# Optimization experiments

Hardware: AMD Instinct MI355X
Metric: run time of the kernel (lower is better)

Reference implementation:

```python
import jax, jax.numpy as jnp
import numpy as np

T_STEPS = 100
T_EMB = 16
EPS = 1e-8


def sin_emb(t, dim):
    # sinusoidal_time_embedding: [cos(t*f), sin(t*f)] with f = exp(-log(1e4)*i/half)
    half = dim // 2
    freqs = jnp.exp(-jnp.log(jnp.float32(10000.0)) * jnp.arange(half, dtype=jnp.float32) / half)
    a = t.astype(jnp.float32)[:, None] * freqs[None, :]
    return jnp.concatenate([jnp.cos(a), jnp.sin(a)], axis=-1)


def lstm_layer(x_tbf, W_ih, W_hh, b):
    # x_tbf: [T, B, F]; torch gate order i, f, g, o
    B = x_tbf.shape[1]
    H = W_hh.shape[1]

    def step(carry, x_t):
        h, c = carry
        g = x_t @ W_ih.T + h @ W_hh.T + b
        i, f, gg, o = jnp.split(g, 4, axis=-1)
        c = jax.nn.sigmoid(f) * c + jax.nn.sigmoid(i) * jnp.tanh(gg)
        h = jax.nn.sigmoid(o) * jnp.tanh(c)
        return (h, c), h

    z = jnp.zeros((B, H), x_tbf.dtype)
    (h, c), ys = jax.lax.scan(step, (z, z), x_tbf)
    return ys, h


def _forward(x_hist, x_future, y0, turb_idx, pred_steps, init_noise, turb_emb,
             W_ih0, W_hh0, b_ih0, b_hh0, W_ih1, W_hh1, b_ih1, b_hh1,
             W1, b1, W2, b2, W3, b3):
    betas = jnp.linspace(1e-4, 0.02, T_STEPS).astype(jnp.float32)
    alphas = 1.0 - betas
    alpha_bars = jnp.cumprod(alphas)

    B = x_hist.shape[0]
    emb = turb_emb[turb_idx]  # [B, E]
    eh = jnp.broadcast_to(emb[:, None, :], (B, x_hist.shape[1], emb.shape[1]))
    ef = jnp.broadcast_to(emb[:, None, :], (B, x_future.shape[1], emb.shape[1]))
    xh = jnp.concatenate([x_hist, eh], axis=-1).transpose(1, 0, 2)    # [T_in, B, F+E]
    xf = jnp.concatenate([x_future, ef], axis=-1).transpose(1, 0, 2)  # [P, B, exo+E]

    ys0, _ = lstm_layer(xh, W_ih0, W_hh0, b_ih0 + b_hh0)
    _, enc_out = lstm_layer(ys0, W_ih1, W_hh1, b_ih1 + b_hh1)         # [B, H] = h[-1]

    def mlp(x):
        h = jax.nn.relu(x @ W1.T + b1)
        h = jax.nn.relu(h @ W2.T + b2)
        return h @ W3.T + b3

    def ar_step(prev_y, xs):
        exo_t, step, y_init = xs
        cond = jnp.concatenate([enc_out, exo_t, prev_y], axis=1)  # [B, cond_dim]
        h_e = sin_emb(jnp.full((B,), step), T_EMB)

        def dstep(y, t):
            t_e = sin_emb(jnp.full((B,), t), T_EMB)
            eps_hat = mlp(jnp.concatenate([cond, y, t_e, h_e], axis=1))  # [B,1]
            b_t, a_t, ab_t = betas[t], alphas[t], alpha_bars[t]
            pred_x0 = (y - jnp.sqrt(1.0 - ab_t) * eps_hat) / (jnp.sqrt(ab_t) + EPS)
            mean = (y - b_t / (jnp.sqrt(1.0 - ab_t) + EPS) * eps_hat) / (jnp.sqrt(a_t) + EPS)
            # eval mode -> deterministic sampling: posterior noise term is zero
            return jnp.where(t == 0, pred_x0, mean), None

        y, _ = jax.lax.scan(dstep, y_init, jnp.arange(T_STEPS - 1, -1, -1))
        return y, y[:, 0]

    _, seq = jax.lax.scan(ar_step, y0, (xf, jnp.arange(pred_steps), init_noise))
    return seq.T[:, :, None]  # [B, pred_steps, 1]


def setup_inputs() -> dict:
    key = jax.random.key(0)
    ks = list(jax.random.split(key, 24))
    kit = iter(ks)
    B, T_IN, F_IN, EXO, EMB, PRED, HID, NTURB = 1024, 96, 8, 6, 16, 8, 128, 100
    in0 = F_IN + EMB                 # 24
    cond_dim = HID + EXO + EMB + 1   # 151
    in_mlp = cond_dim + 1 + T_EMB + T_EMB  # 184

    def nrm(shape, s=0.05):
        return jax.random.normal(next(kit), shape, jnp.float32) * s

    return {
        'x_hist': jax.random.normal(next(kit), (B, T_IN, F_IN), jnp.float32),
        'x_future': jax.random.normal(next(kit), (B, PRED, EXO), jnp.float32),
        'y0': jnp.zeros((B, 1), jnp.float32),
        'turb_idx': jax.random.randint(next(kit), (B,), 0, NTURB),
        'pred_steps': PRED,
        'init_noise': jax.random.normal(next(kit), (PRED, B, 1), jnp.float32),
        'turb_emb': nrm((NTURB, EMB), 0.1),
        'W_ih0': nrm((4 * HID, in0)), 'W_hh0': nrm((4 * HID, HID)),
        'b_ih0': jnp.zeros((4 * HID,), jnp.float32), 'b_hh0': jnp.zeros((4 * HID,), jnp.float32),
        'W_ih1': nrm((4 * HID, HID)), 'W_hh1': nrm((4 * HID, HID)),
        'b_ih1': jnp.zeros((4 * HID,), jnp.float32), 'b_hh1': jnp.zeros((4 * HID,), jnp.float32),
        'W1': nrm((HID, in_mlp)), 'b1': jnp.zeros((HID,), jnp.float32),
        'W2': nrm((HID, HID)), 'b2': jnp.zeros((HID,), jnp.float32),
        'W3': nrm((1, HID)), 'b3': jnp.zeros((1,), jnp.float32),
    }


def reference(x_hist, x_future, y0, turb_idx, pred_steps, init_noise, turb_emb,
              W_ih0, W_hh0, b_ih0, b_hh0, W_ih1, W_hh1, b_ih1, b_hh1,
              W1, b1, W2, b2, W3, b3):
    return _forward(x_hist, x_future, y0, turb_idx, pred_steps, init_noise, turb_emb,
                    W_ih0, W_hh0, b_ih0, b_hh0, W_ih1, W_hh1, b_ih1, b_hh1,
                    W1, b1, W2, b2, W3, b3)
```

## Files before the change

### kernel.cpp

```cpp
#include <hip/hip_runtime.h>
#include <hip/hip_fp16.h>
#include <stdint.h>


typedef __attribute__((ext_vector_type(2))) _Float16 half2_t;
typedef __attribute__((ext_vector_type(8))) _Float16 v8h;
typedef __attribute__((ext_vector_type(4))) float v4f;

#define DEV __device__ __forceinline__

DEV void barrier_lds() {
  asm volatile("s_waitcnt lgkmcnt(0)\ns_barrier" ::: "memory");
}

DEV uint32_t pack2f(float a, float b) {
  __half ha = __float2half_rn(a), hb = __float2half_rn(b);
  return (uint32_t)__half_as_ushort(ha) | ((uint32_t)__half_as_ushort(hb) << 16);
}

DEV float fast_ex2(float x) {
#if __has_builtin(__builtin_amdgcn_exp2f)
  return __builtin_amdgcn_exp2f(x);
#else
  return exp2f(x);
#endif
}
DEV float fast_rcp(float x) {
#if __has_builtin(__builtin_amdgcn_rcpf)
  return __builtin_amdgcn_rcpf(x);
#else
  return 1.f / x;
#endif
}
DEV float sigm(float x) { return fast_rcp(1.f + fast_ex2(-1.4426950408889634f * x)); }
DEV float tanh_f(float x) {
  return 2.f * fast_rcp(1.f + fast_ex2(-2.8853900817779268f * x)) - 1.f;
}

DEV uint32_t pk_add(uint32_t a, uint32_t b) {
  return __builtin_bit_cast(uint32_t,
      __builtin_bit_cast(half2_t, a) + __builtin_bit_cast(half2_t, b));
}

DEV uint32_t pk_fma(uint32_t w, uint32_t y, uint32_t b) {
  return __builtin_bit_cast(uint32_t,
      __builtin_bit_cast(half2_t, w) * __builtin_bit_cast(half2_t, y) +
      __builtin_bit_cast(half2_t, b));
}

DEV uint32_t pk_relufma(uint32_t w, uint32_t y, uint32_t b) {
  half2_t r = __builtin_bit_cast(half2_t, w) * __builtin_bit_cast(half2_t, y) +
              __builtin_bit_cast(half2_t, b);
  half2_t z = {(_Float16)0.f, (_Float16)0.f};
#if __has_builtin(__builtin_elementwise_max)
  r = __builtin_elementwise_max(r, z);
#else
  uint32_t u = __builtin_bit_cast(uint32_t, r);
  uint32_t mask = ((u >> 15) & 1u) * 0xFFFFu | ((u >> 31) & 1u) * 0xFFFF0000u;
  r = __builtin_bit_cast(half2_t, u & ~mask);
#endif
  return __builtin_bit_cast(uint32_t, r);
}

DEV uint32_t cvtpk(float y) {
#if __has_builtin(__builtin_amdgcn_cvt_pkrtz)
  return __builtin_bit_cast(uint32_t, __builtin_amdgcn_cvt_pkrtz(y, y));
#else
  return pack2f(y, y);
#endif
}

static constexpr size_t OFF_XH  = 0;
static constexpr size_t OFF_W0  = 4718592;
static constexpr size_t OFF_BS0 = 4882432;
static constexpr size_t OFF_W1L = 4884480;
static constexpr size_t OFF_BS1 = 5146624;
static constexpr size_t OFF_W2P = 5148672;
static constexpr size_t OFF_ENC = 5181440;
static constexpr size_t OFF_YS0 = 5705728;
static constexpr size_t OFF_BASES = 0;
static constexpr size_t OFF_TPROJ = 2097152;
static constexpr size_t OFF_CC    = 2122752;
static constexpr size_t OFF_W1YP  = 2123584;
static constexpr size_t OFF_W150P = 2123840;

__global__ void k_prep_xh(const float* __restrict__ xh, const int* __restrict__ tix,
                          const float* __restrict__ temb, uint32_t* __restrict__ out) {
  int idx = blockIdx.x * 256 + threadIdx.x;
  if (idx >= 96 * 1024 * 12) return;
  int m = idx % 12;
  int tb = idx / 12;
  int b = tb & 1023, t = tb >> 10;
  int k0 = 2 * m, k1 = k0 + 1;
  float v0 = (k0 < 8) ? xh[(b * 96 + t) * 8 + k0] : temb[tix[b] * 16 + (k0 - 8)];
  float v1 = (k1 < 8) ? xh[(b * 96 + t) * 8 + k1] : temb[tix[b] * 16 + (k1 - 8)];
  out[idx] = pack2f(v0, v1);
}

__global__ void k_prep_w(const float* __restrict__ Wih0, const float* __restrict__ Whh0,
                         const float* __restrict__ bih0, const float* __restrict__ bhh0,
                         const float* __restrict__ Wih1, const float* __restrict__ Whh1,
                         const float* __restrict__ bih1, const float* __restrict__ bhh1,
                         const float* __restrict__ W2,
                         uint32_t* __restrict__ w0p, uint32_t* __restrict__ w1p,
                         uint32_t* __restrict__ w2p, float* __restrict__ bs0,
                         float* __restrict__ bs1) {
  int idx = blockIdx.x * 256 + threadIdx.x;
  if (idx < 40960) {
    int w = idx / 5120;
    int r = idx % 5120;
    int T = r / 1280; r %= 1280;
    int f = r / 256;  r %= 256;
    int l = r >> 2, c = r & 3;
    int m = l & 15, qf = l >> 4;
    int g = (m & 3) * 128 + w * 16 + (m >> 2) * 4 + T;
    int k0 = f * 32 + qf * 8 + 2 * c, k1 = k0 + 1;
    float a = (k0 < 24) ? Wih0[g * 24 + k0] : ((k0 < 152) ? Whh0[g * 128 + k0 - 24] : 0.f);
    float b = (k1 < 24) ? Wih0[g * 24 + k1] : ((k1 < 152) ? Whh0[g * 128 + k1 - 24] : 0.f);
    w0p[idx] = pack2f(a, b);
  } else if (idx < 106496) {
    int i = idx - 40960;
    int w = i / 8192;
    int r = i % 8192;
    int T = r / 2048; r %= 2048;
    int f = r / 256;  r %= 256;
    int l = r >> 2, c = r & 3;
    int m = l & 15, qf = l >> 4;
    int g = (m & 3) * 128 + w * 16 + (m >> 2) * 4 + T;
    int k0 = f * 32 + qf * 8 + 2 * c, k1 = k0 + 1;
    float a = (k0 < 128) ? Wih1[g * 128 + k0] : Whh1[g * 128 + k0 - 128];
    float b = (k1 < 128) ? Wih1[g * 128 + k1] : Whh1[g * 128 + k1 - 128];
    w1p[i] = pack2f(a, b);
  } else if (idx < 114688) {
    int i = idx - 106496;
    w2p[i] = pack2f(W2[2 * i], W2[2 * i + 1]);
  } else if (idx < 115200) {
    int i = idx - 114688;
    bs0[i] = bih0[i] + bhh0[i];
  } else if (idx < 115712) {
    int i = idx - 115200;
    bs1[i] = bih1[i] + bhh1[i];
  }
}

__global__ __launch_bounds__(512, 2) void k_lstm0(const uint32_t* __restrict__ xh16,
                                                  const uint32_t* __restrict__ w0A,
                                                  const float* __restrict__ bs0,
                                                  __half* __restrict__ ys0) {
  __shared__ __align__(16) __half inb[2][16][160];
  const int tid = threadIdx.x;
  const int w = tid >> 6, l = tid & 63;
  const int n = l & 15, ql = l >> 4;
  const int ju = w * 16 + ql * 4;
  const int bbase = blockIdx.x * 16;

  uint4 Af[4][5];
#pragma unroll
  for (int T = 0; T < 4; T++)
#pragma unroll
    for (int f = 0; f < 5; f++)
      Af[T][f] = ((const uint4*)w0A)[((w * 4 + T) * 5 + f) * 64 + l];
  float bias[4][4];
#pragma unroll
  for (int T = 0; T < 4; T++)
#pragma unroll
    for (int r = 0; r < 4; r++) bias[T][r] = bs0[r * 128 + ju + T];

  for (int i = tid; i < 2560; i += 512) ((uint32_t*)inb)[i] = 0u;
  __syncthreads();
  if (tid < 192) {
    int b = tid / 12, m = tid % 12;
    ((uint32_t*)&inb[0][b][0])[m] = xh16[(0 * 1024 + bbase + b) * 12 + m];
  }
  float cst[4] = {0.f, 0.f, 0.f, 0.f};
  __syncthreads();

  for (int t = 0; t < 96; t++) {
    const int cur = t & 1, nxt = cur ^ 1;
    uint32_t sx = 0;
    int sb = 0, sm = 0;
    if (t < 95 && tid < 192) {
      sb = tid / 12; sm = tid % 12;
      sx = xh16[((t + 1) * 1024 + bbase + sb) * 12 + sm];
    }
    v4f acc[4];
#pragma unroll
    for (int T = 0; T < 4; T++) acc[T] = (v4f){0.f, 0.f, 0.f, 0.f};
#pragma unroll
    for (int f = 0; f < 5; f++) {
      uint4 bu = *(const uint4*)&inb[cur][n][f * 32 + ql * 8];
      v8h Bv = __builtin_bit_cast(v8h, bu);
#pragma unroll
      for (int T = 0; T < 4; T++)
        acc[T] = __builtin_amdgcn_mfma_f32_16x16x32_f16(
            __builtin_bit_cast(v8h, Af[T][f]), Bv, acc[T], 0, 0, 0);
    }
    float hv[4];
#pragma unroll
    for (int T = 0; T < 4; T++) {
      float gi = acc[T][0] + bias[T][0];
      float gf = acc[T][1] + bias[T][1];
      float gg = acc[T][2] + bias[T][2];
      float go = acc[T][3] + bias[T][3];
      float c = sigm(gf) * cst[T] + sigm(gi) * tanh_f(gg);
      cst[T] = c;
      hv[T] = sigm(go) * tanh_f(c);
    }
    uint32_t h01 = pack2f(hv[0], hv[1]), h23 = pack2f(hv[2], hv[3]);
    *(uint2*)&inb[nxt][n][24 + ju] = make_uint2(h01, h23);
    *(uint2*)((__half*)ys0 + (size_t)(t * 1024 + bbase + n) * 128 + ju) = make_uint2(h01, h23);
    if (t < 95 && tid < 192) ((uint32_t*)&inb[nxt][sb][0])[sm] = sx;
    barrier_lds();
  }
}

__global__ __launch_bounds__(512, 2) void k_lstm1(const uint32_t* __restrict__ ys0u,
                                                  const uint32_t* __restrict__ w1A,
                                                  const float* __restrict__ bs1,
                                                  float* __restrict__ enc) {
  __shared__ __align__(16) __half inb[2][16][264];
  const int tid = threadIdx.x;
  const int w = tid >> 6, l = tid & 63;
  const int n = l & 15, ql = l >> 4;
  const int ju = w * 16 + ql * 4;
  const int bbase = blockIdx.x * 16;
  const int sb = tid >> 5, sc = tid & 31;

  uint4 Af[4][8];
#pragma unroll
  for (int T = 0; T < 4; T++)
#pragma unroll
    for (int f = 0; f < 8; f++)
      Af[T][f] = ((const uint4*)w1A)[((w * 4 + T) * 8 + f) * 64 + l];
  float bias[4][4];
#pragma unroll
  for (int T = 0; T < 4; T++)
#pragma unroll
    for (int r = 0; r < 4; r++) bias[T][r] = bs1[r * 128 + ju + T];

  for (int i = tid; i < 4224; i += 512) ((uint32_t*)inb)[i] = 0u;
  __syncthreads();
  {
    uint2 v = ((const uint2*)ys0u)[(size_t)(0 * 1024 + bbase + sb) * 32 + sc];
    *(uint2*)&inb[0][sb][sc * 4] = v;
  }
  float cst[4] = {0.f, 0.f, 0.f, 0.f};
  __syncthreads();

  for (int t = 0; t < 96; t++) {
    const int cur = t & 1, nxt = cur ^ 1;
    uint2 sv = make_uint2(0u, 0u);
    if (t < 95)
      sv = ((const uint2*)ys0u)[(size_t)((t + 1) * 1024 + bbase + sb) * 32 + sc];
    v4f acc[4];
#pragma unroll
    for (int T = 0; T < 4; T++) acc[T] = (v4f){0.f, 0.f, 0.f, 0.f};
#pragma unroll
    for (int f = 0; f < 8; f++) {
      uint4 bu = *(const uint4*)&inb[cur][n][f * 32 + ql * 8];
      v8h Bv = __builtin_bit_cast(v8h, bu);
#pragma unroll
      for (int T = 0; T < 4; T++)
        acc[T] = __builtin_amdgcn_mfma_f32_16x16x32_f16(
            __builtin_bit_cast(v8h, Af[T][f]), Bv, acc[T], 0, 0, 0);
    }
    float hv[4];
#pragma unroll
    for (int T = 0; T < 4; T++) {
      float gi = acc[T][0] + bias[T][0];
      float gf = acc[T][1] + bias[T][1];
      float gg = acc[T][2] + bias[T][2];
      float go = acc[T][3] + bias[T][3];
      float c = sigm(gf) * cst[T] + sigm(gi) * tanh_f(gg);
      cst[T] = c;
      hv[T] = sigm(go) * tanh_f(c);
    }
    *(uint2*)&inb[nxt][n][128 + ju] = make_uint2(pack2f(hv[0], hv[1]), pack2f(hv[2], hv[3]));
    if (t < 95) *(uint2*)&inb[nxt][sb][sc * 4] = sv;
    if (t == 95)
      *(float4*)&enc[(size_t)(bbase + n) * 128 + ju] = make_float4(hv[0], hv[1], hv[2], hv[3]);
    barrier_lds();
  }
}

__global__ void k_prep_diff(const float* __restrict__ enc, const float* __restrict__ W1,
                            const float* __restrict__ b1, const float* __restrict__ xfut,
                            const float* __restrict__ temb, const int* __restrict__ tix,
                            __half* __restrict__ baseS, __half* __restrict__ tprojG,
                            float2* __restrict__ ccG, uint32_t* __restrict__ w1ypG,
                            uint32_t* __restrict__ w150pG) {
  const int k = threadIdx.x;
  const int b = blockIdx.x;
  if (b < 1024) {
    __shared__ float encL[128];
    __shared__ float embL[16];
    __shared__ float te8[8][16];
    encL[k] = enc[b * 128 + k];
    if (k < 16) embL[k] = temb[tix[b] * 16 + k];
    {
      int s = k >> 4, i = k & 15;
      float f = expf(-logf(10000.f) * (float)(i & 7) / 8.f);
      float a = (float)s * f;
      te8[s][i] = (i < 8) ? cosf(a) : sinf(a);
    }
    __syncthreads();
    const float* wr = W1 + k * 184;
    float base0 = b1[k];
#pragma unroll 8
    for (int j = 0; j < 128; j++) base0 += wr[j] * encL[j];
#pragma unroll
    for (int i = 0; i < 16; i++) base0 += wr[134 + i] * embL[i];
    for (int s = 0; s < 8; s++) {
      float v = base0;
#pragma unroll
      for (int c = 0; c < 6; c++) v += wr[128 + c] * xfut[(b * 8 + s) * 6 + c];
#pragma unroll
      for (int i = 0; i < 16; i++) v += wr[168 + i] * te8[s][i];
      baseS[(b * 8 + s) * 128 + k] = __float2half_rn(v);
    }
  } else {
    __shared__ float teL[100][16];
    for (int p = k; p < 1600; p += 128) {
      int tt = p >> 4, i = p & 15;
      float f = expf(-logf(10000.f) * (float)(i & 7) / 8.f);
      float a = (float)tt * f;
      teL[tt][i] = (i < 8) ? cosf(a) : sinf(a);
    }
    __syncthreads();
    const float* wr = W1 + k * 184;
    float wte[16];
#pragma unroll
    for (int i = 0; i < 16; i++) wte[i] = wr[152 + i];
    for (int tt = 0; tt < 100; tt++) {
      float sv = 0.f;
#pragma unroll
      for (int i = 0; i < 16; i++) sv += wte[i] * teL[tt][i];
      tprojG[tt * 128 + k] = __float2half_rn(sv);
    }
    if (k < 100) {
      float ab = 1.f, beta = 0.f;
      for (int i = 0; i <= k; i++) {
        beta = 1e-4f + (0.02f - 1e-4f) * (float)i / 99.f;
        ab *= (1.f - beta);
      }
      float cs, cd;
      if (k == 0) { cs = sqrtf(1.f - ab); cd = 1.f / (sqrtf(ab) + 1e-8f); }
      else { cs = beta / (sqrtf(1.f - ab) + 1e-8f); cd = 1.f / (sqrtf(1.f - beta) + 1e-8f); }
      ccG[k] = make_float2(cs, cd);
    }
    if (k < 64) {
      w1ypG[k]  = pack2f(W1[(2 * k) * 184 + 151], W1[(2 * k + 1) * 184 + 151]);
      w150pG[k] = pack2f(W1[(2 * k) * 184 + 150], W1[(2 * k + 1) * 184 + 150]);
    }
  }
}

__global__ __launch_bounds__(128, 1) void k_diff(
    const float* __restrict__ y0, const float* __restrict__ noise,
    const uint32_t* __restrict__ baseS, const uint32_t* __restrict__ tprojG,
    const float2* __restrict__ ccG, const uint32_t* __restrict__ w1ypG,
    const uint32_t* __restrict__ w150pG, const uint32_t* __restrict__ w2p,
    const float* __restrict__ b2, const float* __restrict__ W3,
    const float* __restrict__ b3, float* __restrict__ out) {
  __shared__ __align__(16) uint32_t tprojL[100 * 64];
  __shared__ float2 ccL[100];
  __shared__ float partL[2][2][16];
  const int tid = threadIdx.x;
  const int w = tid >> 6, l = tid & 63;
  const int m = l & 15, q = l >> 4;
  const int bbase = blockIdx.x * 16;
  const int b = bbase + m;

  for (int i = tid; i < 1600; i += 128)
    ((uint4*)tprojL)[i] = ((const uint4*)tprojG)[i];
  for (int i = tid; i < 100; i += 128) ccL[i] = ccG[i];

  uint4 w1yp4[4], w150p4[4];
#pragma unroll
  for (int f = 0; f < 4; f++) {
    w1yp4[f]  = ((const uint4*)w1ypG)[f * 4 + q];
    w150p4[f] = ((const uint4*)w150pG)[f * 4 + q];
  }
  uint4 Wf[4][4];
  const uint4* w2u4 = (const uint4*)w2p;
#pragma unroll
  for (int j = 0; j < 4; j++)
#pragma unroll
    for (int f = 0; f < 4; f++)
      Wf[j][f] = w2u4[((w * 4 + j) * 16 + m) * 16 + f * 4 + q];
  v4f b2v4[4];
  float4 w3v4[4];
#pragma unroll
  for (int nt = 0; nt < 4; nt++) {
    float4 bv = *(const float4*)&b2[(w * 4 + nt) * 16 + q * 4];
    b2v4[nt] = (v4f){bv.x, bv.y, bv.z, bv.w};
    w3v4[nt] = *(const float4*)&W3[(w * 4 + nt) * 16 + q * 4];
  }
  const float b3v = b3[0];
  float py = y0[b];
  __syncthreads();

  for (int s = 0; s < 8; s++) {
    uint32_t bph[16];
    {
      uint32_t pyP = cvtpk(py);
#pragma unroll
      for (int f = 0; f < 4; f++) {
        uint4 ba = ((const uint4*)baseS)[(b * 8 + s) * 16 + f * 4 + q];
        bph[f * 4 + 0] = pk_fma(w150p4[f].x, pyP, ba.x);
        bph[f * 4 + 1] = pk_fma(w150p4[f].y, pyP, ba.y);
        bph[f * 4 + 2] = pk_fma(w150p4[f].z, pyP, ba.z);
        bph[f * 4 + 3] = pk_fma(w150p4[f].w, pyP, ba.w);
      }
    }
    float y = noise[s * 1024 + b];

    uint32_t bt0[16], bt1[16];
#pragma unroll
    for (int f = 0; f < 4; f++) {
      uint4 tv = *(const uint4*)&tprojL[99 * 64 + f * 16 + q * 4];
      bt0[f * 4 + 0] = pk_add(bph[f * 4 + 0], tv.x);
      bt0[f * 4 + 1] = pk_add(bph[f * 4 + 1], tv.y);
      bt0[f * 4 + 2] = pk_add(bph[f * 4 + 2], tv.z);
      bt0[f * 4 + 3] = pk_add(bph[f * 4 + 3], tv.w);
    }
    float2 ccv = ccL[99];

#define DIFF_STEP(T_, BT_, BTN_, BUF_)                                          \
    {                                                                           \
      uint32_t yP = cvtpk(y);                                                   \
      v4f acc[4];                                                               \
      _Pragma("unroll")                                                         \
      for (int f = 0; f < 4; f++) {                                             \
        uint4 au;                                                               \
        au.x = pk_relufma(w1yp4[f].x, yP, BT_[f * 4 + 0]);                      \
        au.y = pk_relufma(w1yp4[f].y, yP, BT_[f * 4 + 1]);                      \
        au.z = pk_relufma(w1yp4[f].z, yP, BT_[f * 4 + 2]);                      \
        au.w = pk_relufma(w1yp4[f].w, yP, BT_[f * 4 + 3]);                      \
        v8h Hb = __builtin_bit_cast(v8h, au);                                   \
        _Pragma("unroll")                                                       \
        for (int j = 0; j < 4; j++) {                                           \
          v4f c = (f == 0) ? b2v4[j] : acc[j];                                  \
          acc[j] = __builtin_amdgcn_mfma_f32_16x16x32_f16(                      \
              __builtin_bit_cast(v8h, Wf[j][f]), Hb, c, 0, 0, 0);               \
        }                                                                       \
      }                                                                         \
      const int tn_ = ((T_) > 0) ? (T_) - 1 : 0;                                \
      _Pragma("unroll")                                                         \
      for (int f = 0; f < 4; f++) {                                             \
        uint4 tv = *(const uint4*)&tprojL[tn_ * 64 + f * 16 + q * 4];           \
        BTN_[f * 4 + 0] = pk_add(bph[f * 4 + 0], tv.x);                         \
        BTN_[f * 4 + 1] = pk_add(bph[f * 4 + 1], tv.y);                         \
        BTN_[f * 4 + 2] = pk_add(bph[f * 4 + 2], tv.z);                         \
        BTN_[f * 4 + 3] = pk_add(bph[f * 4 + 3], tv.w);                         \
      }                                                                         \
      float2 ccn = ccL[tn_];                                                    \
      float local = 0.f;                                                        \
      _Pragma("unroll")                                                         \
      for (int j = 0; j < 4; j++) {                                             \
        local += w3v4[j].x * fmaxf(acc[j][0], 0.f);                             \
        local += w3v4[j].y * fmaxf(acc[j][1], 0.f);                             \
        local += w3v4[j].z * fmaxf(acc[j][2], 0.f);                             \
        local += w3v4[j].w * fmaxf(acc[j][3], 0.f);                             \
      }                                                                         \
      local += __shfl_xor(local, 16, 64);                                       \
      local += __shfl_xor(local, 32, 64);                                       \
      if (l < 16) partL[BUF_][w][l] = local;                                    \
      barrier_lds();                                                            \
      float eps = local + partL[BUF_][1 - w][m] + b3v;                          \
      y = (y - ccv.x * eps) * ccv.y;                                            \
      ccv = ccn;                                                                \
    }

    for (int tt = 0; tt < 50; tt++) {
      const int t = 99 - 2 * tt;
      DIFF_STEP(t, bt0, bt1, 0)
      DIFF_STEP(t - 1, bt1, bt0, 1)
    }
#undef DIFF_STEP

    if (w == 0 && l < 16) out[(bbase + l) * 8 + s] = y;
    py = y;
  }
}

extern "C" void kernel_launch(void* const* d_in, const int* in_sizes, int n_in,
                              void* d_out, int out_size, void* d_ws, size_t ws_size,
                              hipStream_t stream) {
  const float* x_hist    = (const float*)d_in[0];
  const float* x_future  = (const float*)d_in[1];
  const float* y0        = (const float*)d_in[2];
  const int*   turb_idx  = (const int*)d_in[3];
  const float* init_noise = (const float*)d_in[5];
  const float* turb_emb  = (const float*)d_in[6];
  const float* W_ih0     = (const float*)d_in[7];
  const float* W_hh0     = (const float*)d_in[8];
  const float* b_ih0     = (const float*)d_in[9];
  const float* b_hh0     = (const float*)d_in[10];
  const float* W_ih1     = (const float*)d_in[11];
  const float* W_hh1     = (const float*)d_in[12];
  const float* b_ih1     = (const float*)d_in[13];
  const float* b_hh1     = (const float*)d_in[14];
  const float* W1        = (const float*)d_in[15];
  const float* b1        = (const float*)d_in[16];
  const float* W2        = (const float*)d_in[17];
  const float* b2        = (const float*)d_in[18];
  const float* W3        = (const float*)d_in[19];
  const float* b3        = (const float*)d_in[20];

  char* ws = (char*)d_ws;
  uint32_t* xh16 = (uint32_t*)(ws + OFF_XH);
  uint32_t* w0p  = (uint32_t*)(ws + OFF_W0);
  float*    bs0  = (float*)(ws + OFF_BS0);
  uint32_t* w1p  = (uint32_t*)(ws + OFF_W1L);
  float*    bs1  = (float*)(ws + OFF_BS1);
  uint32_t* w2p  = (uint32_t*)(ws + OFF_W2P);
  float*    encf = (float*)(ws + OFF_ENC);
  __half*   ys0h = (__half*)(ws + OFF_YS0);
  __half*   baseS  = (__half*)(ws + OFF_BASES);
  __half*   tprojG = (__half*)(ws + OFF_TPROJ);
  float2*   ccG    = (float2*)(ws + OFF_CC);
  uint32_t* w1ypG  = (uint32_t*)(ws + OFF_W1YP);
  uint32_t* w150pG = (uint32_t*)(ws + OFF_W150P);

  k_prep_xh<<<4608, 256, 0, stream>>>(x_hist, turb_idx, turb_emb, xh16);
  k_prep_w<<<452, 256, 0, stream>>>(W_ih0, W_hh0, b_ih0, b_hh0,
                                    W_ih1, W_hh1, b_ih1, b_hh1,
                                    W2, w0p, w1p, w2p, bs0, bs1);
  k_lstm0<<<64, 512, 0, stream>>>(xh16, w0p, bs0, ys0h);
  k_lstm1<<<64, 512, 0, stream>>>((const uint32_t*)ys0h, w1p, bs1, encf);
  k_prep_diff<<<1025, 128, 0, stream>>>(encf, W1, b1, x_future, turb_emb, turb_idx,
                                        baseS, tprojG, ccG, w1ypG, w150pG);
  k_diff<<<64, 128, 0, stream>>>(y0, init_noise, (const uint32_t*)baseS,
                                 (const uint32_t*)tprojG, ccG, w1ypG, w150pG,
                                 w2p, b2, W3, b3, (float*)d_out);
}
```

Before: 689.3 us.

## Process two batch tiles per block and interleave their diffusion steps

Each k_diff block now handles 32 batch rows as two 16-row groups (A and B) instead of one. The MFMA issue of one group is interleaved with the epilogue and cross-wave reduction of the other, so the serial dependency chain of each diffusion step overlaps with independent work, and one barrier covers both groups per step. The grid is halved from 64 to 32 blocks, which cuts parallelism across CUs and raises register pressure in exchange for better latency hiding per block.

```diff
diff --git a/kernel.cpp b/kernel.cpp
--- a/kernel.cpp
+++ b/kernel.cpp
@@ -364,12 +364,12 @@
     const float* __restrict__ b3, float* __restrict__ out) {
   __shared__ __align__(16) uint32_t tprojL[100 * 64];
   __shared__ float2 ccL[100];
-  __shared__ float partL[2][2][16];
+  __shared__ float partL[2][2][2][16];
   const int tid = threadIdx.x;
   const int w = tid >> 6, l = tid & 63;
   const int m = l & 15, q = l >> 4;
-  const int bbase = blockIdx.x * 16;
-  const int b = bbase + m;
+  const int bbase = blockIdx.x * 32;
+  const int bA = bbase + m, bB = bbase + 16 + m;
 
   for (int i = tid; i < 1600; i += 128)
     ((uint4*)tprojL)[i] = ((const uint4*)tprojG)[i];
@@ -397,91 +397,122 @@
     w3v4[nt] = *(const float4*)&W3[(w * 4 + nt) * 16 + q * 4];
   }
   const float b3v = b3[0];
-  float py = y0[b];
+  float pyA = y0[bA], pyB = y0[bB];
   __syncthreads();
 
-  for (int s = 0; s < 8; s++) {
-    uint32_t bph[16];
-    {
-      uint32_t pyP = cvtpk(py);
-#pragma unroll
-      for (int f = 0; f < 4; f++) {
-        uint4 ba = ((const uint4*)baseS)[(b * 8 + s) * 16 + f * 4 + q];
-        bph[f * 4 + 0] = pk_fma(w150p4[f].x, pyP, ba.x);
-        bph[f * 4 + 1] = pk_fma(w150p4[f].y, pyP, ba.y);
-        bph[f * 4 + 2] = pk_fma(w150p4[f].z, pyP, ba.z);
-        bph[f * 4 + 3] = pk_fma(w150p4[f].w, pyP, ba.w);
-      }
-    }
-    float y = noise[s * 1024 + b];
-
-    uint32_t bt0[16], bt1[16];
-#pragma unroll
-    for (int f = 0; f < 4; f++) {
-      uint4 tv = *(const uint4*)&tprojL[99 * 64 + f * 16 + q * 4];
-      bt0[f * 4 + 0] = pk_add(bph[f * 4 + 0], tv.x);
-      bt0[f * 4 + 1] = pk_add(bph[f * 4 + 1], tv.y);
-      bt0[f * 4 + 2] = pk_add(bph[f * 4 + 2], tv.z);
-      bt0[f * 4 + 3] = pk_add(bph[f * 4 + 3], tv.w);
-    }
-    float2 ccv = ccL[99];
-
-#define DIFF_STEP(T_, BT_, BTN_, BUF_)                                          \
-    {                                                                           \
-      uint32_t yP = cvtpk(y);                                                   \
-      v4f acc[4];                                                               \
-      _Pragma("unroll")                                                         \
-      for (int f = 0; f < 4; f++) {                                             \
-        uint4 au;                                                               \
-        au.x = pk_relufma(w1yp4[f].x, yP, BT_[f * 4 + 0]);                      \
-        au.y = pk_relufma(w1yp4[f].y, yP, BT_[f * 4 + 1]);                      \
-        au.z = pk_relufma(w1yp4[f].z, yP, BT_[f * 4 + 2]);                      \
-        au.w = pk_relufma(w1yp4[f].w, yP, BT_[f * 4 + 3]);                      \
-        v8h Hb = __builtin_bit_cast(v8h, au);                                   \
-        _Pragma("unroll")                                                       \
-        for (int j = 0; j < 4; j++) {                                           \
-          v4f c = (f == 0) ? b2v4[j] : acc[j];                                  \
-          acc[j] = __builtin_amdgcn_mfma_f32_16x16x32_f16(                      \
-              __builtin_bit_cast(v8h, Wf[j][f]), Hb, c, 0, 0, 0);               \
-        }                                                                       \
-      }                                                                         \
-      const int tn_ = ((T_) > 0) ? (T_) - 1 : 0;                                \
-      _Pragma("unroll")                                                         \
-      for (int f = 0; f < 4; f++) {                                             \
-        uint4 tv = *(const uint4*)&tprojL[tn_ * 64 + f * 16 + q * 4];           \
-        BTN_[f * 4 + 0] = pk_add(bph[f * 4 + 0], tv.x);                         \
-        BTN_[f * 4 + 1] = pk_add(bph[f * 4 + 1], tv.y);                         \
-        BTN_[f * 4 + 2] = pk_add(bph[f * 4 + 2], tv.z);                         \
-        BTN_[f * 4 + 3] = pk_add(bph[f * 4 + 3], tv.w);                         \
-      }                                                                         \
-      float2 ccn = ccL[tn_];                                                    \
-      float local = 0.f;                                                        \
+#define ISSUE(ACC_, BPH_, TV_, YP_)                                             \
+    _Pragma("unroll")                                                           \
+    for (int f = 0; f < 4; f++) {                                               \
+      uint4 au;                                                                 \
+      au.x = pk_relufma(w1yp4[f].x, YP_, pk_add(BPH_[f * 4 + 0], TV_[f].x));    \
+      au.y = pk_relufma(w1yp4[f].y, YP_, pk_add(BPH_[f * 4 + 1], TV_[f].y));    \
+      au.z = pk_relufma(w1yp4[f].z, YP_, pk_add(BPH_[f * 4 + 2], TV_[f].z));    \
+      au.w = pk_relufma(w1yp4[f].w, YP_, pk_add(BPH_[f * 4 + 3], TV_[f].w));    \
+      v8h Hb = __builtin_bit_cast(v8h, au);                                     \
       _Pragma("unroll")                                                         \
       for (int j = 0; j < 4; j++) {                                             \
-        local += w3v4[j].x * fmaxf(acc[j][0], 0.f);                             \
-        local += w3v4[j].y * fmaxf(acc[j][1], 0.f);                             \
-        local += w3v4[j].z * fmaxf(acc[j][2], 0.f);                             \
-        local += w3v4[j].w * fmaxf(acc[j][3], 0.f);                             \
+        v4f c = (f == 0) ? b2v4[j] : ACC_[j];                                   \
+        ACC_[j] = __builtin_amdgcn_mfma_f32_16x16x32_f16(                       \
+            __builtin_bit_cast(v8h, Wf[j][f]), Hb, c, 0, 0, 0);                 \
       }                                                                         \
-      local += __shfl_xor(local, 16, 64);                                       \
-      local += __shfl_xor(local, 32, 64);                                       \
-      if (l < 16) partL[BUF_][w][l] = local;                                    \
-      barrier_lds();                                                            \
-      float eps = local + partL[BUF_][1 - w][m] + b3v;                          \
-      y = (y - ccv.x * eps) * ccv.y;                                            \
-      ccv = ccn;                                                                \
-    }
-
-    for (int tt = 0; tt < 50; tt++) {
-      const int t = 99 - 2 * tt;
-      DIFF_STEP(t, bt0, bt1, 0)
-      DIFF_STEP(t - 1, bt1, bt0, 1)
-    }
-#undef DIFF_STEP
-
-    if (w == 0 && l < 16) out[(bbase + l) * 8 + s] = y;
-    py = y;
-  }
+    }
+
+#define EPILOG(ACC_, LOCAL_)                                                    \
+    {                                                                           \
+      float p01 = w3v4[0].x * fmaxf(ACC_[0][0], 0.f) +                          \
+                  w3v4[0].y * fmaxf(ACC_[0][1], 0.f) +                          \
+                  w3v4[1].x * fmaxf(ACC_[1][0], 0.f) +                          \
+                  w3v4[1].y * fmaxf(ACC_[1][1], 0.f);                           \
+      float p23 = w3v4[0].z * fmaxf(ACC_[0][2], 0.f) +                          \
+                  w3v4[0].w * fmaxf(ACC_[0][3], 0.f) +                          \
+                  w3v4[1].z * fmaxf(ACC_[1][2], 0.f) +                          \
+                  w3v4[1].w * fmaxf(ACC_[1][3], 0.f);                           \
+      float p45 = w3v4[2].x * fmaxf(ACC_[2][0], 0.f) +                          \
+                  w3v4[2].y * fmaxf(ACC_[2][1], 0.f) +                          \
+                  w3v4[3].x * fmaxf(ACC_[3][0], 0.f) +                          \
+                  w3v4[3].y * fmaxf(ACC_[3][1], 0.f);                           \
+      float p67 = w3v4[2].z * fmaxf(ACC_[2][2], 0.f) +                          \
+                  w3v4[2].w * fmaxf(ACC_[2][3], 0.f) +                          \
+                  w3v4[3].z * fmaxf(ACC_[3][2], 0.f) +                          \
+                  w3v4[3].w * fmaxf(ACC_[3][3], 0.f);                           \
+      LOCAL_ = (p01 + p23) + (p45 + p67);                                       \
+      LOCAL_ += __shfl_xor(LOCAL_, 16, 64);                                     \
+      LOCAL_ += __shfl_xor(LOCAL_, 32, 64);                                     \
+    }
+
+  int buf = 0;
+  for (int s = 0; s < 8; s++) {
+    uint32_t bphA[16], bphB[16];
+    {
+      uint32_t pyPA = cvtpk(pyA), pyPB = cvtpk(pyB);
+#pragma unroll
+      for (int f = 0; f < 4; f++) {
+        uint4 ba = ((const uint4*)baseS)[(bA * 8 + s) * 16 + f * 4 + q];
+        uint4 bb = ((const uint4*)baseS)[(bB * 8 + s) * 16 + f * 4 + q];
+        bphA[f * 4 + 0] = pk_fma(w150p4[f].x, pyPA, ba.x);
+        bphA[f * 4 + 1] = pk_fma(w150p4[f].y, pyPA, ba.y);
+        bphA[f * 4 + 2] = pk_fma(w150p4[f].z, pyPA, ba.z);
+        bphA[f * 4 + 3] = pk_fma(w150p4[f].w, pyPA, ba.w);
+        bphB[f * 4 + 0] = pk_fma(w150p4[f].x, pyPB, bb.x);
+        bphB[f * 4 + 1] = pk_fma(w150p4[f].y, pyPB, bb.y);
+        bphB[f * 4 + 2] = pk_fma(w150p4[f].z, pyPB, bb.z);
+        bphB[f * 4 + 3] = pk_fma(w150p4[f].w, pyPB, bb.w);
+      }
+    }
+    float yA = noise[s * 1024 + bA];
+    float yB = noise[s * 1024 + bB];
+
+    uint4 tv[4];
+#pragma unroll
+    for (int f = 0; f < 4; f++)
+      tv[f] = *(const uint4*)&tprojL[99 * 64 + f * 16 + q * 4];
+    float2 ccv = ccL[99];
+
+    v4f accB[4];
+    {
+      uint32_t yPB = cvtpk(yB);
+      ISSUE(accB, bphB, tv, yPB)
+    }
+
+    for (int t = 99; t >= 0; t--) {
+      v4f accA[4];
+      {
+        uint32_t yPA = cvtpk(yA);
+        ISSUE(accA, bphA, tv, yPA)
+      }
+      float localB;
+      EPILOG(accB, localB)
+      if (l < 16) partL[buf][1][w][l] = localB;
+      float localA;
+      EPILOG(accA, localA)
+      if (l < 16) partL[buf][0][w][l] = localA;
+      const int tn = (t > 0) ? t - 1 : 0;
+      uint4 tvn[4];
+#pragma unroll
+      for (int f = 0; f < 4; f++)
+        tvn[f] = *(const uint4*)&tprojL[tn * 64 + f * 16 + q * 4];
+      float2 ccn = ccL[tn];
+      barrier_lds();
+      float epsA = localA + partL[buf][0][1 - w][m] + b3v;
+      yA = (yA - ccv.x * epsA) * ccv.y;
+      float epsB = localB + partL[buf][1][1 - w][m] + b3v;
+      yB = (yB - ccv.x * epsB) * ccv.y;
+      if (t > 0) {
+        uint32_t yPB = cvtpk(yB);
+        ISSUE(accB, bphB, tvn, yPB)
+      }
+#pragma unroll
+      for (int f = 0; f < 4; f++) tv[f] = tvn[f];
+      ccv = ccn;
+      buf ^= 1;
+    }
+    if (w == 0 && l < 16) out[(bbase + l) * 8 + s] = yA;
+    if (w == 1 && l < 16) out[(bbase + 16 + l) * 8 + s] = yB;
+    pyA = yA;
+    pyB = yB;
+  }
+#undef ISSUE
+#undef EPILOG
 }
 
 extern "C" void kernel_launch(void* const* d_in, const int* in_sizes, int n_in,
@@ -531,7 +562,7 @@
   k_lstm1<<<64, 512, 0, stream>>>((const uint32_t*)ys0h, w1p, bs1, encf);
   k_prep_diff<<<1025, 128, 0, stream>>>(encf, W1, b1, x_future, turb_emb, turb_idx,
                                         baseS, tprojG, ccG, w1ypG, w150pG);
-  k_diff<<<64, 128, 0, stream>>>(y0, init_noise, (const uint32_t*)baseS,
+  k_diff<<<32, 128, 0, stream>>>(y0, init_noise, (const uint32_t*)baseS,
                                  (const uint32_t*)tprojG, ccG, w1ypG, w150pG,
                                  w2p, b2, W3, b3, (float*)d_out);
 }
```

After: 1.131 ms. 64.1% more time.
